# Kernel optimization log

Hardware: AMD Instinct MI355X
Metric: run time of the kernel (lower is better)

The kernel has to match this reference:

```python
import jax, jax.numpy as jnp
import numpy as np

D = 1024
H = 16
HD = D // H  # 64


def setup_inputs() -> dict:
    key = jax.random.key(0)
    ks = jax.random.split(key, 10)
    s = 0.02
    return {
        "x": jax.random.normal(ks[0], (2, 2048, D), dtype=jnp.float32),
        "rel_bias": jax.random.normal(ks[1], (H, 2048, 2048), dtype=jnp.float32),
        "Wq": jax.random.normal(ks[2], (D, D), dtype=jnp.float32) * s,
        "bq": jnp.zeros((D,), dtype=jnp.float32),
        "Wk": jax.random.normal(ks[3], (D, D), dtype=jnp.float32) * s,
        "bk": jnp.zeros((D,), dtype=jnp.float32),
        "Wv": jax.random.normal(ks[4], (D, D), dtype=jnp.float32) * s,
        "bv": jnp.zeros((D,), dtype=jnp.float32),
        "Wo": jax.random.normal(ks[5], (D, D), dtype=jnp.float32) * s,
        "bo": jnp.zeros((D,), dtype=jnp.float32),
    }


def reference(x, rel_bias, Wq, bq, Wk, bk, Wv, bv, Wo, bo):
    B, L, _ = x.shape
    # QKV projections -> [B, H, L, HD]
    def proj(W, b):
        return (x @ W.T + b).reshape(B, L, H, HD).transpose(0, 2, 1, 3)
    q = proj(Wq, bq)
    k = proj(Wk, bk)
    v = proj(Wv, bv)
    scale = 1.0 / jnp.sqrt(jnp.float32(HD))
    scores = jnp.einsum("bhqd,bhkd->bhqk", q, k) * scale + rel_bias[None]
    attn = jax.nn.softmax(scores, axis=-1)  # dropout p=0 -> identity
    out = jnp.einsum("bhqk,bhkd->bhqd", attn, v)
    out = out.transpose(0, 2, 1, 3).reshape(B, L, H * HD)
    return out @ Wo.T + bo
```

## Files before the change

### kernel.cpp

```cpp
#include <hip/hip_runtime.h>


typedef __attribute__((ext_vector_type(8))) short bf16x8;
typedef __attribute__((ext_vector_type(4))) float f32x4;
typedef __attribute__((ext_vector_type(8))) unsigned short u16x8;
using u16 = unsigned short;

#define MFMA16(a, b, c) __builtin_amdgcn_mfma_f32_16x16x32_bf16((a), (b), (c), 0, 0, 0)
#define LOG2E 1.44269504088896f
#define QSCALE (0.125f * 1.44269504088896f)

__device__ __forceinline__ u16 f2bf(float f) {
  union { float f; unsigned int u; } v; v.f = f;
  unsigned int r = v.u + 0x7FFFu + ((v.u >> 16) & 1u);
  return (u16)(r >> 16);
}

__device__ __forceinline__ unsigned cvt_pk_bf16(float lo, float hi) {
  unsigned r;
  asm volatile("v_cvt_pk_bf16_f32 %0, %1, %2" : "=v"(r) : "v"(lo), "v"(hi));
  return r;
}

__device__ __forceinline__ void g2lds16(const void* gsrc, void* ldst) {
  __builtin_amdgcn_global_load_lds(
      (const __attribute__((address_space(1))) unsigned int*)gsrc,
      (__attribute__((address_space(3))) unsigned int*)ldst, 16, 0, 0);
}

__global__ __launch_bounds__(256) void cvt_all(
    const float* __restrict__ x, const float* __restrict__ wq,
    const float* __restrict__ wk, const float* __restrict__ wv,
    const float* __restrict__ wo, u16* __restrict__ xb,
    u16* __restrict__ w1b, u16* __restrict__ wob) {
  int bid = blockIdx.x, tid = threadIdx.x;
  const float* src; u16* dst; int i;
  if (bid < 2048)      { src = x;  dst = xb;            i = bid * 256 + tid; }
  else if (bid < 2560) { src = wq; dst = w1b;           i = (bid - 2048) * 256 + tid; }
  else if (bid < 3072) { src = wk; dst = w1b + (1<<20); i = (bid - 2560) * 256 + tid; }
  else if (bid < 3584) { src = wv; dst = w1b + (2<<20); i = (bid - 3072) * 256 + tid; }
  else                 { src = wo; dst = wob;           i = (bid - 3584) * 256 + tid; }
  const float4* s = (const float4*)src;
  float4 a = s[2 * i], b = s[2 * i + 1];
  u16x8 o;
  o[0] = f2bf(a.x); o[1] = f2bf(a.y); o[2] = f2bf(a.z); o[3] = f2bf(a.w);
  o[4] = f2bf(b.x); o[5] = f2bf(b.y); o[6] = f2bf(b.z); o[7] = f2bf(b.w);
  ((u16x8*)dst)[i] = o;
}

template <int MODE>
__global__ __launch_bounds__(256, 2) void gemm_bt(
    const u16* __restrict__ A, const u16* __restrict__ B,
    u16* __restrict__ qp, u16* __restrict__ kp, u16* __restrict__ vp,
    const float* __restrict__ b0, const float* __restrict__ b1,
    const float* __restrict__ b2, float* __restrict__ outp,
    const float* __restrict__ bo) {
  __shared__ __align__(16) u16 lA[128 * 64];
  __shared__ __align__(16) u16 lB[128 * 64];
  const int tid = threadIdx.x;
  const int lane = tid & 63, wid = tid >> 6;
  const int g = lane >> 4, cc = lane & 15;
  const int wr = wid >> 1, wc = wid & 1;
  const int m0 = blockIdx.y * 128, n0 = blockIdx.x * 128;
  f32x4 acc[4][4] = {};
  for (int kt = 0; kt < 16; ++kt) {
    const int kof = kt * 64;
#pragma unroll
    for (int i = 0; i < 4; ++i) {
      int cid = i * 256 + tid;
      int row = cid >> 3;
      int col = (cid & 7) * 8;
      g2lds16(A + (size_t)(m0 + row) * 1024 + kof + col, &lA[(i * 256 + wid * 64) * 8]);
      g2lds16(B + (size_t)(n0 + row) * 1024 + kof + col, &lB[(i * 256 + wid * 64) * 8]);
    }
    __syncthreads();
#pragma unroll
    for (int kc = 0; kc < 2; ++kc) {
      bf16x8 af[4], bfr[4];
#pragma unroll
      for (int mf = 0; mf < 4; ++mf)
        af[mf] = *(const bf16x8*)&lA[(wr * 64 + mf * 16 + cc) * 64 + kc * 32 + g * 8];
#pragma unroll
      for (int nf = 0; nf < 4; ++nf)
        bfr[nf] = *(const bf16x8*)&lB[(wc * 64 + nf * 16 + cc) * 64 + kc * 32 + g * 8];
#pragma unroll
      for (int mf = 0; mf < 4; ++mf)
#pragma unroll
        for (int nf = 0; nf < 4; ++nf)
          acc[mf][nf] = MFMA16(af[mf], bfr[nf], acc[mf][nf]);
    }
    __syncthreads();
  }
#pragma unroll
  for (int mf = 0; mf < 4; ++mf) {
#pragma unroll
    for (int nf = 0; nf < 4; ++nf) {
      int n = n0 + wc * 64 + nf * 16 + cc;
      if (MODE == 0) {
        int which = n >> 10;
        int nn = n & 1023;
        const float* bp = which == 0 ? b0 : (which == 1 ? b1 : b2);
        float bias = bp[nn];
        int h = nn >> 6, hd = nn & 63;
        int mb = m0 + wr * 64 + mf * 16 + g * 4;
        int bb = mb >> 11, ll0 = mb & 2047;
        if (which == 2) {
          ushort4 pk4;
          pk4.x = f2bf(acc[mf][nf][0] + bias);
          pk4.y = f2bf(acc[mf][nf][1] + bias);
          pk4.z = f2bf(acc[mf][nf][2] + bias);
          pk4.w = f2bf(acc[mf][nf][3] + bias);
          *(ushort4*)&vp[(((size_t)(bb * 16 + h)) * 64 + hd) * 2048 + ll0] = pk4;
        } else {
          u16* dp = which == 0 ? qp : kp;
#pragma unroll
          for (int r = 0; r < 4; ++r) {
            float val = acc[mf][nf][r] + bias;
            if (which == 0) val *= QSCALE;
            dp[(((size_t)(bb * 16 + h)) * 2048 + ll0 + r) * 64 + hd] = f2bf(val);
          }
        }
      } else {
        float bias = bo[n];
#pragma unroll
        for (int r = 0; r < 4; ++r) {
          int m = m0 + wr * 64 + mf * 16 + g * 4 + r;
          outp[(size_t)m * 1024 + n] = acc[mf][nf][r] + bias;
        }
      }
    }
  }
}

__global__ __launch_bounds__(512, 4) void attn_kernel(
    const u16* __restrict__ qm, const u16* __restrict__ km,
    const u16* __restrict__ vtm, const float* __restrict__ bias,
    u16* __restrict__ aout) {
  __shared__ __align__(16) u16 lK[4096];
  __shared__ __align__(16) u16 lV[4096];
  __shared__ __align__(16) u16 plds[8192];
  const int tid = threadIdx.x;
  const int lane = tid & 63, wid = tid >> 6;
  const int g = lane >> 4, cc = lane & 15;
  const int lin = blockIdx.x;
  const int xcd = lin & 7, j = lin >> 3;
  const int h = xcd * 2 + (j >> 5);
  const int rem = j & 31;
  const int b = rem >> 4, qb = rem & 15;
  const int q0 = qb * 128;
  const size_t bh = (size_t)b * 16 + h;
  const u16* kg = km + bh * 2048 * 64;
  const u16* vg = vtm + bh * 64 * 2048;
  const u16* qbase = qm + (bh * 2048 + q0 + wid * 16) * 64;
  const float* brow = bias + ((size_t)h * 2048 + q0 + wid * 16 + cc) * 2048;
  u16* plw = plds + wid * 1024;

  bf16x8 qf0 = *(const bf16x8*)&qbase[(size_t)cc * 64 + g * 8];
  bf16x8 qf1 = *(const bf16x8*)&qbase[(size_t)cc * 64 + 32 + g * 8];
  f32x4 o[4] = {};
  float mrow = -3.0e38f, lrow = 0.f;

#define STAGE_TILE(gbase, rs, ldst)                                            \
  {                                                                            \
    int row = tid >> 3, pcol = tid & 7;                                        \
    int lcol = pcol ^ (row & 7);                                               \
    g2lds16((gbase) + (size_t)row * (rs) + lcol * 8, (ldst) + tid * 8);        \
  }

  float4 bA[4];
  STAGE_TILE(kg, 64, (u16*)lK)
  __builtin_amdgcn_sched_barrier(0);
#pragma unroll
  for (int kb = 0; kb < 4; ++kb)
    bA[kb] = *(const float4*)(brow + kb * 16 + g * 4);
  __builtin_amdgcn_sched_barrier(0);
  asm volatile("s_waitcnt vmcnt(4)" ::: "memory");
  __builtin_amdgcn_sched_barrier(0);

#define ATTN_STEP(kt_, DOPRE)                                                  \
  {                                                                            \
    const int k0 = (kt_) * 64;                                                 \
    __builtin_amdgcn_s_barrier();     \
    __builtin_amdgcn_sched_barrier(0);                                         \
                               \
    STAGE_TILE(vg + k0, 2048, (u16*)lV)                                        \
    __builtin_amdgcn_sched_barrier(0);                                         \
                       \
    f32x4 s[4];                                                                \
    _Pragma("unroll") for (int kb = 0; kb < 4; ++kb) {                         \
      int row = kb * 16 + cc;                                                  \
      bf16x8 ka = *(const bf16x8*)&lK[row * 64 + ((0 + g) ^ (cc & 7)) * 8];    \
      bf16x8 kbf = *(const bf16x8*)&lK[row * 64 + ((4 + g) ^ (cc & 7)) * 8];   \
      f32x4 z = {};                                                            \
      z = MFMA16(ka, qf0, z);                                                  \
      z = MFMA16(kbf, qf1, z);                                                 \
      s[kb] = z;                                                               \
    }                                                                          \
    _Pragma("unroll") for (int kb = 0; kb < 4; ++kb) {                         \
      s[kb][0] = fmaf(bA[kb].x, LOG2E, s[kb][0]);                              \
      s[kb][1] = fmaf(bA[kb].y, LOG2E, s[kb][1]);                              \
      s[kb][2] = fmaf(bA[kb].z, LOG2E, s[kb][2]);                              \
      s[kb][3] = fmaf(bA[kb].w, LOG2E, s[kb][3]);                              \
    }                                                                          \
                             \
    float rmax = s[0][0];                                                      \
    _Pragma("unroll") for (int kb = 0; kb < 4; ++kb)                           \
        _Pragma("unroll") for (int r = 0; r < 4; ++r)                          \
            rmax = fmaxf(rmax, s[kb][r]);                                      \
    rmax = fmaxf(rmax, __shfl_xor(rmax, 16, 64));                              \
    rmax = fmaxf(rmax, __shfl_xor(rmax, 32, 64));                              \
    float mnew = fmaxf(mrow, rmax);                                            \
    float sc = __builtin_amdgcn_exp2f(mrow - mnew);                            \
    mrow = mnew;                                                               \
    float psum = 0.f;                                                          \
    _Pragma("unroll") for (int kb = 0; kb < 4; ++kb)                           \
        _Pragma("unroll") for (int r = 0; r < 4; ++r) {                        \
      s[kb][r] = __builtin_amdgcn_exp2f(s[kb][r] - mrow);                      \
      psum += s[kb][r];                                                        \
    }                                                                          \
    psum += __shfl_xor(psum, 16, 64);                                          \
    psum += __shfl_xor(psum, 32, 64);                                          \
    lrow = lrow * sc + psum;                                                   \
    float scb[4];                                                              \
    _Pragma("unroll") for (int r = 0; r < 4; ++r)                              \
        scb[r] = __shfl(sc, (lane & 48) | (((lane >> 4) & 3) * 4 + r), 64);    \
    _Pragma("unroll") for (int td = 0; td < 4; ++td)                           \
        _Pragma("unroll") for (int r = 0; r < 4; ++r) o[td][r] *= scb[r];      \
                \
    __builtin_amdgcn_sched_barrier(0);                                         \
    asm volatile("s_waitcnt vmcnt(0)" ::: "memory");                           \
    __builtin_amdgcn_sched_barrier(0);                                         \
    __builtin_amdgcn_s_barrier();                                              \
    __builtin_amdgcn_sched_barrier(0);                                         \
    if (DOPRE) {                                                               \
                \
      STAGE_TILE(kg + (size_t)(k0 + 64) * 64, 64, (u16*)lK)                    \
      __builtin_amdgcn_sched_barrier(0);                                       \
      _Pragma("unroll") for (int kb = 0; kb < 4; ++kb)                         \
          bA[kb] = *(const float4*)(brow + k0 + 64 + kb * 16 + g * 4);         \
      __builtin_amdgcn_sched_barrier(0);                                       \
    }                                                                          \
                                \
    _Pragma("unroll") for (int kb = 0; kb < 4; ++kb) {                         \
      unsigned lo = cvt_pk_bf16(s[kb][0], s[kb][1]);                           \
      unsigned hi = cvt_pk_bf16(s[kb][2], s[kb][3]);                           \
      int ch = (kb * 4 + g) ^ ((cc & 7) << 1);                                 \
      ((uint2*)plw)[cc * 16 + ch] = make_uint2(lo, hi);                        \
    }                                                                          \
    bf16x8 pf0 = *(const bf16x8*)&plw[cc * 64 + (((2 * g) ^ ((cc & 7) << 1)) * 4)]; \
    bf16x8 pf1 = *(const bf16x8*)&plw[cc * 64 + (((8 + 2 * g) ^ ((cc & 7) << 1)) * 4)]; \
    _Pragma("unroll") for (int td = 0; td < 4; ++td) {                         \
      int row = td * 16 + cc;                                                  \
      bf16x8 va = *(const bf16x8*)&lV[row * 64 + ((0 + g) ^ (cc & 7)) * 8];    \
      bf16x8 vb = *(const bf16x8*)&lV[row * 64 + ((4 + g) ^ (cc & 7)) * 8];    \
      o[td] = MFMA16(pf0, va, o[td]);                                          \
      o[td] = MFMA16(pf1, vb, o[td]);                                          \
    }                                                                          \
                \
    __builtin_amdgcn_sched_barrier(0);                                         \
    if (DOPRE) { asm volatile("s_waitcnt vmcnt(4)" ::: "memory"); }            \
    else       { asm volatile("s_waitcnt vmcnt(0)" ::: "memory"); }            \
    __builtin_amdgcn_sched_barrier(0);                                         \
  }

  for (int kt = 0; kt < 31; ++kt) {
    ATTN_STEP(kt, 1)
  }
  ATTN_STEP(31, 0)
#undef ATTN_STEP
#undef STAGE_TILE

  float linv = 1.0f / lrow;
  float lb[4];
#pragma unroll
  for (int r = 0; r < 4; ++r)
    lb[r] = __shfl(linv, (lane & 48) | (((lane >> 4) & 3) * 4 + r), 64);
#pragma unroll
  for (int td = 0; td < 4; ++td)
#pragma unroll
    for (int r = 0; r < 4; ++r) {
      float val = o[td][r] * lb[r];
      int qg = q0 + wid * 16 + g * 4 + r;
      aout[((size_t)b * 2048 + qg) * 1024 + h * 64 + td * 16 + cc] = f2bf(val);
    }
}

extern "C" void kernel_launch(void* const* d_in, const int* in_sizes, int n_in,
                              void* d_out, int out_size, void* d_ws, size_t ws_size,
                              hipStream_t stream) {
  const float* x  = (const float*)d_in[0];
  const float* rb = (const float*)d_in[1];
  const float* Wq = (const float*)d_in[2];
  const float* bq = (const float*)d_in[3];
  const float* Wk = (const float*)d_in[4];
  const float* bk = (const float*)d_in[5];
  const float* Wv = (const float*)d_in[6];
  const float* bv = (const float*)d_in[7];
  const float* Wo = (const float*)d_in[8];
  const float* bo = (const float*)d_in[9];
  float* out = (float*)d_out;
  char* ws = (char*)d_ws;

  u16* xb   = (u16*)(ws);
  u16* W1b  = (u16*)(ws + (8 << 20));
  u16* Wob  = (u16*)(ws + (14 << 20));
  u16* qb   = (u16*)(ws + (16 << 20));
  u16* kb2  = (u16*)(ws + (24 << 20));
  u16* vtb  = (u16*)(ws + (32 << 20));
  u16* aout = xb;

  cvt_all<<<4096, 256, 0, stream>>>(x, Wq, Wk, Wv, Wo, xb, W1b, Wob);
  gemm_bt<0><<<dim3(24, 32), 256, 0, stream>>>(xb, W1b, qb, kb2, vtb, bq, bk, bv,
                                               nullptr, nullptr);
  attn_kernel<<<512, 512, 0, stream>>>(qb, kb2, vtb, rb, aout);
  gemm_bt<1><<<dim3(8, 32), 256, 0, stream>>>(aout, Wob, nullptr, nullptr, nullptr,
                                              nullptr, nullptr, nullptr, out, bo);
}
```

Measured before the change: 176.7 us.

## Double-buffer K/V tiles in LDS and prefetch bias two tiles ahead

The attention kernel now keeps two LDS buffers each for K and V. The next K/V tile is staged at the start of each step, and bias is loaded two tiles ahead using alternating register sets. This drops the mid-step wait plus barrier and leaves one barrier per step, so global loads can overlap the QK, softmax and PV work. In exchange it doubles K/V LDS use, which may lower occupancy under launch_bounds(512,4), and it uses more registers for the second bias set.

```diff
diff --git a/kernel.cpp b/kernel.cpp
--- a/kernel.cpp
+++ b/kernel.cpp
@@ -136,8 +136,8 @@
     const u16* __restrict__ qm, const u16* __restrict__ km,
     const u16* __restrict__ vtm, const float* __restrict__ bias,
     u16* __restrict__ aout) {
-  __shared__ __align__(16) u16 lK[4096];
-  __shared__ __align__(16) u16 lV[4096];
+  __shared__ __align__(16) u16 lK[2][4096];
+  __shared__ __align__(16) u16 lV[2][4096];
   __shared__ __align__(16) u16 plds[8192];
   const int tid = threadIdx.x;
   const int lane = tid & 63, wid = tid >> 6;
@@ -167,40 +167,46 @@
     g2lds16((gbase) + (size_t)row * (rs) + lcol * 8, (ldst) + tid * 8);        \
   }
 
-  float4 bA[4];
-  STAGE_TILE(kg, 64, (u16*)lK)
+  float4 bA[4], bB[4];
+  STAGE_TILE(kg, 64, (u16*)lK[0])
+  STAGE_TILE(vg, 2048, (u16*)lV[0])
   __builtin_amdgcn_sched_barrier(0);
 #pragma unroll
-  for (int kb = 0; kb < 4; ++kb)
+  for (int kb = 0; kb < 4; ++kb) {
     bA[kb] = *(const float4*)(brow + kb * 16 + g * 4);
+    bB[kb] = *(const float4*)(brow + 64 + kb * 16 + g * 4);
+  }
   __builtin_amdgcn_sched_barrier(0);
-  asm volatile("s_waitcnt vmcnt(4)" ::: "memory");
+  asm volatile("s_waitcnt vmcnt(8)" ::: "memory");
   __builtin_amdgcn_sched_barrier(0);
-
-#define ATTN_STEP(kt_, DOPRE)                                                  \
+  __builtin_amdgcn_s_barrier();
+  __builtin_amdgcn_sched_barrier(0);
+
+#define ATTN_STEP(kt_, BC, DOSTAGE, DOBIAS)                                    \
   {                                                                            \
     const int k0 = (kt_) * 64;                                                 \
-    __builtin_amdgcn_s_barrier();     \
-    __builtin_amdgcn_sched_barrier(0);                                         \
-                               \
-    STAGE_TILE(vg + k0, 2048, (u16*)lV)                                        \
+    const int P = (kt_) & 1;                                                   \
+    if (DOSTAGE) {                                                             \
+      STAGE_TILE(kg + (size_t)(k0 + 64) * 64, 64, (u16*)lK[P ^ 1])             \
+      STAGE_TILE(vg + (k0 + 64), 2048, (u16*)lV[P ^ 1])                        \
+    }                                                                          \
     __builtin_amdgcn_sched_barrier(0);                                         \
                        \
     f32x4 s[4];                                                                \
     _Pragma("unroll") for (int kb = 0; kb < 4; ++kb) {                         \
       int row = kb * 16 + cc;                                                  \
-      bf16x8 ka = *(const bf16x8*)&lK[row * 64 + ((0 + g) ^ (cc & 7)) * 8];    \
-      bf16x8 kbf = *(const bf16x8*)&lK[row * 64 + ((4 + g) ^ (cc & 7)) * 8];   \
+      bf16x8 ka = *(const bf16x8*)&lK[P][row * 64 + ((0 + g) ^ (cc & 7)) * 8]; \
+      bf16x8 kbf = *(const bf16x8*)&lK[P][row * 64 + ((4 + g) ^ (cc & 7)) * 8];\
       f32x4 z = {};                                                            \
       z = MFMA16(ka, qf0, z);                                                  \
       z = MFMA16(kbf, qf1, z);                                                 \
       s[kb] = z;                                                               \
     }                                                                          \
     _Pragma("unroll") for (int kb = 0; kb < 4; ++kb) {                         \
-      s[kb][0] = fmaf(bA[kb].x, LOG2E, s[kb][0]);                              \
-      s[kb][1] = fmaf(bA[kb].y, LOG2E, s[kb][1]);                              \
-      s[kb][2] = fmaf(bA[kb].z, LOG2E, s[kb][2]);                              \
-      s[kb][3] = fmaf(bA[kb].w, LOG2E, s[kb][3]);                              \
+      s[kb][0] = fmaf(BC[kb].x, LOG2E, s[kb][0]);                              \
+      s[kb][1] = fmaf(BC[kb].y, LOG2E, s[kb][1]);                              \
+      s[kb][2] = fmaf(BC[kb].z, LOG2E, s[kb][2]);                              \
+      s[kb][3] = fmaf(BC[kb].w, LOG2E, s[kb][3]);                              \
     }                                                                          \
                              \
     float rmax = s[0][0];                                                      \
@@ -226,20 +232,12 @@
         scb[r] = __shfl(sc, (lane & 48) | (((lane >> 4) & 3) * 4 + r), 64);    \
     _Pragma("unroll") for (int td = 0; td < 4; ++td)                           \
         _Pragma("unroll") for (int r = 0; r < 4; ++r) o[td][r] *= scb[r];      \
-                \
-    __builtin_amdgcn_sched_barrier(0);                                         \
-    asm volatile("s_waitcnt vmcnt(0)" ::: "memory");                           \
-    __builtin_amdgcn_sched_barrier(0);                                         \
-    __builtin_amdgcn_s_barrier();                                              \
-    __builtin_amdgcn_sched_barrier(0);                                         \
-    if (DOPRE) {                                                               \
-                \
-      STAGE_TILE(kg + (size_t)(k0 + 64) * 64, 64, (u16*)lK)                    \
-      __builtin_amdgcn_sched_barrier(0);                                       \
+            \
+    if (DOBIAS) {                                                              \
       _Pragma("unroll") for (int kb = 0; kb < 4; ++kb)                         \
-          bA[kb] = *(const float4*)(brow + k0 + 64 + kb * 16 + g * 4);         \
-      __builtin_amdgcn_sched_barrier(0);                                       \
-    }                                                                          \
+          BC[kb] = *(const float4*)(brow + k0 + 128 + kb * 16 + g * 4);        \
+    }                                                                          \
+    __builtin_amdgcn_sched_barrier(0);                                         \
                                 \
     _Pragma("unroll") for (int kb = 0; kb < 4; ++kb) {                         \
       unsigned lo = cvt_pk_bf16(s[kb][0], s[kb][1]);                           \
@@ -251,22 +249,26 @@
     bf16x8 pf1 = *(const bf16x8*)&plw[cc * 64 + (((8 + 2 * g) ^ ((cc & 7) << 1)) * 4)]; \
     _Pragma("unroll") for (int td = 0; td < 4; ++td) {                         \
       int row = td * 16 + cc;                                                  \
-      bf16x8 va = *(const bf16x8*)&lV[row * 64 + ((0 + g) ^ (cc & 7)) * 8];    \
-      bf16x8 vb = *(const bf16x8*)&lV[row * 64 + ((4 + g) ^ (cc & 7)) * 8];    \
+      bf16x8 va = *(const bf16x8*)&lV[P][row * 64 + ((0 + g) ^ (cc & 7)) * 8]; \
+      bf16x8 vb = *(const bf16x8*)&lV[P][row * 64 + ((4 + g) ^ (cc & 7)) * 8]; \
       o[td] = MFMA16(pf0, va, o[td]);                                          \
       o[td] = MFMA16(pf1, vb, o[td]);                                          \
     }                                                                          \
-                \
-    __builtin_amdgcn_sched_barrier(0);                                         \
-    if (DOPRE) { asm volatile("s_waitcnt vmcnt(4)" ::: "memory"); }            \
-    else       { asm volatile("s_waitcnt vmcnt(0)" ::: "memory"); }            \
-    __builtin_amdgcn_sched_barrier(0);                                         \
-  }
-
-  for (int kt = 0; kt < 31; ++kt) {
-    ATTN_STEP(kt, 1)
-  }
-  ATTN_STEP(31, 0)
+           \
+    __builtin_amdgcn_sched_barrier(0);                                         \
+    if (DOSTAGE && DOBIAS) { asm volatile("s_waitcnt vmcnt(4)" ::: "memory"); }\
+    else                   { asm volatile("s_waitcnt vmcnt(0)" ::: "memory"); }\
+    __builtin_amdgcn_sched_barrier(0);                                         \
+    if (DOSTAGE) { __builtin_amdgcn_s_barrier(); }                             \
+    __builtin_amdgcn_sched_barrier(0);                                         \
+  }
+
+  for (int kt = 0; kt < 30; kt += 2) {
+    ATTN_STEP(kt, bA, 1, 1)
+    ATTN_STEP(kt + 1, bB, 1, 1)
+  }
+  ATTN_STEP(30, bA, 1, 0)
+  ATTN_STEP(31, bB, 0, 0)
 #undef ATTN_STEP
 #undef STAGE_TILE
 
```

Result: faster. 168.8 us (-4.4%).
